# Kernel tuning notes

Hardware: AMD Instinct MI355X
Metric: run time of the kernel (lower is better)

The kernel has to match this reference:

```python
import jax, jax.numpy as jnp
import numpy as np
from jax import lax

IN_CHANNELS = 4
STEPS_IN_ITR = 3


def one_step_ltm(x, T):
    # x: [B, H, W]; T: [B, 10, H, W] (9 stencil weight planes + bias plane)
    B, H, W = x.shape
    xp = jnp.pad(x, ((0, 0), (1, 1), (1, 1)))
    out = T[:, 9]
    k = 0
    # original ordering: X0..X2 scan row-offset with col-offset 0, X3..X5 col 1, X6..X8 col 2
    for dj in range(3):
        for di in range(3):
            out = out + xp[:, di:di + H, dj:dj + W] * T[:, k]
            k += 1
    return out


def setup_inputs() -> dict:
    key = jax.random.key(0)
    k1, k2, k3 = jax.random.split(key, 3)
    B, Tt, C, H, W = 8, 16, 1, 512, 512
    x = jax.random.uniform(k1, (B, Tt, C, H, W), dtype=jnp.float32)
    # stand-in unet: 3x3 SAME conv, in_channels -> 10
    W_unet = jax.random.normal(k2, (10, IN_CHANNELS, 3, 3), dtype=jnp.float32) * 0.1
    b_unet = jax.random.normal(k3, (10,), dtype=jnp.float32) * 0.1
    return {"x": x, "W_unet": W_unet, "b_unet": b_unet}


def reference(x, W_unet, b_unet):
    B, Tt, C, H, W = x.shape
    x_in = x[:, -IN_CHANNELS:, 0]  # [B, in_channels, H, W]
    T = lax.conv_general_dilated(
        x_in, W_unet, window_strides=(1, 1), padding='SAME',
        dimension_numbers=('NCHW', 'OIHW', 'NCHW')) + b_unet[None, :, None, None]

    xt0 = one_step_ltm(x[:, -1, 0], T)  # stored at t=0 WITHOUT sigmoid (as in original)

    def body(xt, _):
        for _j in range(STEPS_IN_ITR):
            xt = one_step_ltm(xt, T)
            xt = jax.nn.sigmoid(one_step_ltm(xt, T))
        return xt, xt

    _, xs = lax.scan(body, xt0, None, length=Tt - 1)  # [Tt-1, B, H, W]
    seq = jnp.concatenate([xt0[None], xs], axis=0)     # [Tt, B, H, W]
    seq = jnp.transpose(seq, (1, 0, 2, 3))             # [B, Tt, H, W]
    xout = jnp.zeros((B, Tt, C, H, W), dtype=x.dtype).at[:, :, 0].set(seq)
    return xout
```

## Files before the change

### kernel.cpp

```cpp
#include <hip/hip_runtime.h>
#include <hip/hip_fp16.h>
#include <math.h>

#define Bd 8
#define Td 16
#define Hd 512
#define Wd 512
#define HWc (Hd * Wd)
#define NPIX (Bd * HWc)

#define VTW 128
#define VTH 16
#define VRW 130
#define VRH 18
#define VP  132
#define VTHR 512

#define WCR 128
#define WCC 64
#define WH  6
#define WTR 140
#define WTC 76
#define WLP 77
#define WTHR 1024
#define WRPG 11
#define WNG 13

__global__ __launch_bounds__(VTHR, 4)
void conv_step0_kernel(const float* __restrict__ x,
                       const float* __restrict__ Wu,
                       const float* __restrict__ bu,
                       __half2* __restrict__ T,
                       float* __restrict__ out) {
    __shared__ __align__(16) float sX[4][VRH][VP];

    int bx  = blockIdx.x;
    int b   = bx >> 7;
    int rem = bx & 127;
    int by  = rem >> 2;
    int bc  = rem & 3;
    int i0  = by * VTH;
    int j0  = bc * VTW;

    const float* xb = x + ((size_t)b * Td + 12) * HWc;
    int tid = threadIdx.x;

    for (int idx = tid; idx < 4 * VRH * VRW; idx += VTHR) {
        int ch = idx / (VRH * VRW);
        int r2 = idx - ch * (VRH * VRW);
        int r  = r2 / VRW;
        int c  = r2 - r * VRW;
        int gi = i0 + r - 1, gj = j0 + c - 1;
        float v = 0.0f;
        if ((unsigned)gi < (unsigned)Hd && (unsigned)gj < (unsigned)Wd)
            v = xb[(size_t)ch * HWc + gi * Wd + gj];
        sX[ch][r][c] = v;
    }
    __syncthreads();

    int tx = tid & 63;
    int ty = tid >> 6;

    float t00[10], t01[10], t10[10], t11[10];
    #pragma unroll
    for (int o = 0; o < 10; ++o) {
        float bv = bu[o];
        t00[o] = bv; t01[o] = bv; t10[o] = bv; t11[o] = bv;
    }

    float w[4][4];
    #pragma unroll
    for (int ch = 0; ch < 4; ++ch) {
        #pragma unroll
        for (int rr = 0; rr < 4; ++rr) {
            const float* rp = &sX[ch][2 * ty + rr][2 * tx];
            float2 a  = *(const float2*)rp;
            float2 b2 = *(const float2*)(rp + 2);
            w[rr][0] = a.x; w[rr][1] = a.y; w[rr][2] = b2.x; w[rr][3] = b2.y;
        }
        #pragma unroll
        for (int kh = 0; kh < 3; ++kh) {
            #pragma unroll
            for (int o = 0; o < 10; ++o) {
                float wt0 = Wu[((o * 4 + ch) * 3 + kh) * 3 + 0];
                float wt1 = Wu[((o * 4 + ch) * 3 + kh) * 3 + 1];
                float wt2 = Wu[((o * 4 + ch) * 3 + kh) * 3 + 2];
                t00[o] += w[kh][0] * wt0 + w[kh][1] * wt1 + w[kh][2] * wt2;
                t01[o] += w[kh][1] * wt0 + w[kh][2] * wt1 + w[kh][3] * wt2;
                t10[o] += w[kh + 1][0] * wt0 + w[kh + 1][1] * wt1 + w[kh + 1][2] * wt2;
                t11[o] += w[kh + 1][1] * wt0 + w[kh + 1][2] * wt1 + w[kh + 1][3] * wt2;
            }
        }
    }

    int gi0 = i0 + 2 * ty;
    int gj0 = j0 + 2 * tx;
    size_t pix0 = (size_t)gi0 * Wd + gj0;
    size_t pix1 = pix0 + Wd;
    __half2* Tb = T + (size_t)b * 5 * HWc;
    #pragma unroll
    for (int q = 0; q < 5; ++q) {
        __half2 a0 = __floats2half2_rn(t00[2 * q], t00[2 * q + 1]);
        __half2 a1 = __floats2half2_rn(t01[2 * q], t01[2 * q + 1]);
        __half2 b0 = __floats2half2_rn(t10[2 * q], t10[2 * q + 1]);
        __half2 b1 = __floats2half2_rn(t11[2 * q], t11[2 * q + 1]);
        uint2 p0, p1;
        p0.x = *(unsigned*)&a0; p0.y = *(unsigned*)&a1;
        p1.x = *(unsigned*)&b0; p1.y = *(unsigned*)&b1;
        *(uint2*)(Tb + (size_t)q * HWc + pix0) = p0;
        *(uint2*)(Tb + (size_t)q * HWc + pix1) = p1;
    }

    float o00 = t00[9], o01 = t01[9], o10 = t10[9], o11 = t11[9];
    #pragma unroll
    for (int dj = 0; dj < 3; ++dj)
        #pragma unroll
        for (int di = 0; di < 3; ++di) {
            int k = dj * 3 + di;
            o00 += w[di][dj]         * t00[k];
            o01 += w[di][dj + 1]     * t01[k];
            o10 += w[di + 1][dj]     * t10[k];
            o11 += w[di + 1][dj + 1] * t11[k];
        }
    float* ob = out + (size_t)b * Td * HWc;
    float2 v0; v0.x = o00; v0.y = o01;
    float2 v1; v1.x = o10; v1.y = o11;
    *(float2*)(ob + pix0) = v0;
    *(float2*)(ob + pix1) = v1;
}

__global__ __launch_bounds__(WTHR, 2)
void fused6_wide_kernel(const float* __restrict__ xin,
                        const __half2* __restrict__ T,
                        float* __restrict__ xout) {
    __shared__ float sA[WTR * WLP];
    __shared__ float sB[WTR * WLP];

    int tile = blockIdx.x;
    int b  = tile >> 5;
    int tr = (tile >> 3) & 3;
    int tc = tile & 7;
    int ri = tr * WCR - WH;
    int rj = tc * WCC - WH;

    const float* xb = xin + (size_t)b * Td * HWc;
    const __half2* Tb = T + (size_t)b * 5 * HWc;
    int tid = threadIdx.x;

    for (int idx = tid; idx < WTR * WTC; idx += WTHR) {
        int r = idx / WTC, c = idx - r * WTC;
        int gi = ri + r, gj = rj + c;
        float v = 0.0f;
        if ((unsigned)gi < (unsigned)Hd && (unsigned)gj < (unsigned)Wd)
            v = xb[gi * Wd + gj];
        sA[r * WLP + c] = v;
    }
    for (int idx = tid; idx < 2 * WTC; idx += WTHR) {
        int r = (idx < WTC) ? 0 : (WTR - 1);
        int c = (idx < WTC) ? idx : idx - WTC;
        sB[r * WLP + c] = 0.0f;
    }
    for (int idx = tid; idx < 2 * WTR; idx += WTHR) {
        int r = (idx < WTR) ? idx : idx - WTR;
        int c = (idx < WTR) ? 0 : (WTC - 1);
        sB[r * WLP + c] = 0.0f;
    }

    int g  = tid / WTC;
    int c  = tid - g * WTC;
    int rs = 1 + g * WRPG;
    bool colint = (c >= 1) && (c <= WTC - 2);
    bool active = (g < WNG) && colint;
    int  gj     = rj + c;
    bool colin  = (unsigned)gj < (unsigned)Wd;

    __half2 treg[WRPG][5];
    #pragma unroll
    for (int jj = 0; jj < WRPG; ++jj) {
        int r  = rs + jj;
        int gi = ri + r;
        bool ok = active && (r <= WTR - 2) && ((unsigned)gi < (unsigned)Hd) && colin;
        #pragma unroll
        for (int q = 0; q < 5; ++q)
            treg[jj][q] = ok ? Tb[(size_t)q * HWc + gi * Wd + gj]
                             : __floats2half2_rn(0.0f, 0.0f);
    }
    __syncthreads();

    float* cur = sA;
    float* nxt = sB;

    #pragma unroll
    for (int s = 1; s <= 6; ++s) {
        if (active) {
            float w00 = cur[(rs - 1) * WLP + c - 1];
            float w01 = cur[(rs - 1) * WLP + c];
            float w02 = cur[(rs - 1) * WLP + c + 1];
            float w10 = cur[rs * WLP + c - 1];
            float w11 = cur[rs * WLP + c];
            float w12 = cur[rs * WLP + c + 1];
            #pragma unroll
            for (int jj = 0; jj < WRPG; ++jj) {
                int r  = rs + jj;
                int r2 = (r + 1 <= WTR - 1) ? (r + 1) : (WTR - 1);
                float w20 = cur[r2 * WLP + c - 1];
                float w21 = cur[r2 * WLP + c];
                float w22 = cur[r2 * WLP + c + 1];

                float2 p0 = __half22float2(treg[jj][0]);
                float2 p1 = __half22float2(treg[jj][1]);
                float2 p2 = __half22float2(treg[jj][2]);
                float2 p3 = __half22float2(treg[jj][3]);
                float2 p4 = __half22float2(treg[jj][4]);

                float a = p4.y
                        + w00 * p0.x + w10 * p0.y + w20 * p1.x
                        + w01 * p1.y + w11 * p2.x + w21 * p2.y
                        + w02 * p3.x + w12 * p3.y + w22 * p4.x;
                if ((s & 1) == 0) a = 1.0f / (1.0f + __expf(-a));

                int gi = ri + r;
                bool rowok = (r <= WTR - 2);
                bool inimg = ((unsigned)gi < (unsigned)Hd) && colin;
                if (rowok) nxt[r * WLP + c] = inimg ? a : 0.0f;

                w00 = w10; w01 = w11; w02 = w12;
                w10 = w20; w11 = w21; w12 = w22;
            }
        }
        __syncthreads();
        float* tmp = cur; cur = nxt; nxt = tmp;
    }

    float* ob = xout + (size_t)b * Td * HWc;
    for (int idx = tid; idx < WCR * WCC; idx += WTHR) {
        int rr = idx >> 6, cc = idx & 63;
        ob[(ri + WH + rr) * Wd + (rj + WH + cc)] = cur[(WH + rr) * WLP + (WH + cc)];
    }
}

extern "C" void kernel_launch(void* const* d_in, const int* in_sizes, int n_in,
                              void* d_out, int out_size, void* d_ws, size_t ws_size,
                              hipStream_t stream) {
    const float* x  = (const float*)d_in[0];
    const float* Wu = (const float*)d_in[1];
    const float* bu = (const float*)d_in[2];
    float* out = (float*)d_out;
    __half2* T = (__half2*)d_ws;

    conv_step0_kernel<<<1024, VTHR, 0, stream>>>(x, Wu, bu, T, out);

    for (int t = 1; t < Td; ++t)
        fused6_wide_kernel<<<256, WTHR, 0, stream>>>(out + (size_t)(t - 1) * HWc, T,
                                                     out + (size_t)t * HWc);
}
```

Measured before the change: 546.8 us.

## Add register-resident lane-shuffle stencil kernel with mixed-precision FMA

```diff
diff --git a/kernel.cpp b/kernel.cpp
--- a/kernel.cpp
+++ b/kernel.cpp
@@ -25,6 +25,44 @@
 #define WTHR 1024
 #define WRPG 11
 #define WNG 13
+
+#define KCR 64
+#define KCC 52
+#define KH  6
+#define KTR 76
+#define KTC 64
+#define KG  7
+#define KR  11
+#define KTHR (KG * 64)
+
+#define FMAMIX_LO(acc, wv, hv) \
+    asm("v_fma_mix_f32 %0, %1, %2, %0 op_sel:[0,0,0] op_sel_hi:[0,1,0]" \
+        : "+v"(acc) : "v"(wv), "v"(hv))
+#define FMAMIX_HI(acc, wv, hv) \
+    asm("v_fma_mix_f32 %0, %1, %2, %0 op_sel:[0,1,0] op_sel_hi:[0,1,0]" \
+        : "+v"(acc) : "v"(wv), "v"(hv))
+
+__device__ __forceinline__ float hi_half_f32(unsigned h) {
+    __half2 hh = *(__half2*)&h;
+    return __half2float(__high2half(hh));
+}
+
+__device__ __forceinline__ float lane_left(float v) {
+#if __has_builtin(__builtin_amdgcn_mov_dpp)
+    return __int_as_float(__builtin_amdgcn_mov_dpp(__float_as_int(v),
+                                                   0x138, 0xf, 0xf, true));
+#else
+    return __shfl_up(v, 1);
+#endif
+}
+__device__ __forceinline__ float lane_right(float v) {
+#if __has_builtin(__builtin_amdgcn_mov_dpp)
+    return __int_as_float(__builtin_amdgcn_mov_dpp(__float_as_int(v),
+                                                   0x130, 0xf, 0xf, true));
+#else
+    return __shfl_down(v, 1);
+#endif
+}
 
 __global__ __launch_bounds__(VTHR, 4)
 void conv_step0_kernel(const float* __restrict__ x,
@@ -129,6 +167,112 @@
     *(float2*)(ob + pix1) = v1;
 }
 
+__global__ __launch_bounds__(KTHR, 2)
+void fused6_lane_kernel(const float* __restrict__ xin,
+                        const __half2* __restrict__ T,
+                        float* __restrict__ xout) {
+    __shared__ float bndF[2][KG][64];
+    __shared__ float bndL[2][KG][64];
+
+    int tile = blockIdx.x;
+    int b   = tile / 80;
+    int rem = tile - b * 80;
+    int tr  = rem / 10;
+    int tc  = rem - tr * 10;
+    int ri  = tr * KCR - KH;
+    int rj  = tc * KCC - KH;
+
+    int tid  = threadIdx.x;
+    int g    = tid >> 6;
+    int lane = tid & 63;
+
+    int  gj     = rj + lane;
+    bool colin  = (unsigned)gj < (unsigned)Wd;
+    bool lanein = (lane >= 1) && (lane <= KTC - 2);
+    int  gjc    = min(max(gj, 0), Wd - 1);
+
+    int rs = 1 + g * KR;
+
+    const float* xb = xin + (size_t)b * Td * HWc;
+    const __half2* Tb = T + (size_t)b * 5 * HWc;
+
+    float xw[KR + 2];
+    #pragma unroll
+    for (int k = 0; k < KR + 2; ++k) {
+        int row = rs - 1 + k;
+        int gi  = ri + row;
+        bool in = ((unsigned)gi < (unsigned)Hd) && colin && (row <= KTR - 1);
+        int gic = min(max(gi, 0), Hd - 1);
+        float v = xb[gic * Wd + gjc];
+        xw[k] = in ? v : 0.0f;
+    }
+
+    unsigned treg[KR][5];
+    #pragma unroll
+    for (int j = 0; j < KR; ++j) {
+        int gi  = ri + rs + j;
+        int gic = min(max(gi, 0), Hd - 1);
+        const unsigned* tp = (const unsigned*)(Tb + gic * Wd + gjc);
+        #pragma unroll
+        for (int q = 0; q < 5; ++q)
+            treg[j][q] = tp[(size_t)q * HWc];
+    }
+
+    int p = 0;
+    #pragma unroll
+    for (int s = 1; s <= 6; ++s) {
+        float pC = xw[0], pL = lane_left(pC), pR = lane_right(pC);
+        float cC = xw[1], cL = lane_left(cC), cR = lane_right(cC);
+        #pragma unroll
+        for (int j = 1; j <= KR; ++j) {
+            float nC = xw[j + 1];
+            float nL = lane_left(nC);
+            float nR = lane_right(nC);
+            unsigned h0 = treg[j - 1][0], h1 = treg[j - 1][1],
+                     h2 = treg[j - 1][2], h3 = treg[j - 1][3],
+                     h4 = treg[j - 1][4];
+            float a = hi_half_f32(h4);
+            FMAMIX_LO(a, pL, h0);
+            FMAMIX_HI(a, cL, h0);
+            FMAMIX_LO(a, nL, h1);
+            FMAMIX_HI(a, pC, h1);
+            FMAMIX_LO(a, cC, h2);
+            FMAMIX_HI(a, nC, h2);
+            FMAMIX_LO(a, pR, h3);
+            FMAMIX_HI(a, cR, h3);
+            FMAMIX_LO(a, nR, h4);
+            if ((s & 1) == 0) a = 1.0f / (1.0f + __expf(-a));
+
+            int row = rs + j - 1;
+            int gi  = ri + row;
+            bool okpix = ((unsigned)gi < (unsigned)Hd) && colin;
+            bool upd   = (row <= KTR - 2) && lanein;
+            float val  = okpix ? a : 0.0f;
+            xw[j] = upd ? val : xw[j];
+
+            pL = cL; pC = cC; pR = cR;
+            cL = nL; cC = nC; cR = nR;
+        }
+        bndF[p][g][lane] = xw[1];
+        bndL[p][g][lane] = xw[KR];
+        __syncthreads();
+        if (g > 0)      xw[0]      = bndL[p][g - 1][lane];
+        if (g < KG - 1) xw[KR + 1] = bndF[p][g + 1][lane];
+        p ^= 1;
+    }
+
+    float* ob = xout + (size_t)b * Td * HWc;
+    bool storec = (lane >= KH) && (lane <= KTC - 1 - KH) && colin;
+    #pragma unroll
+    for (int j = 1; j <= KR; ++j) {
+        int row = rs + j - 1;
+        if (row >= KH && row <= KTR - 1 - KH) {
+            int gi = ri + row;
+            if (storec) ob[gi * Wd + gj] = xw[j];
+        }
+    }
+}
+
 __global__ __launch_bounds__(WTHR, 2)
 void fused6_wide_kernel(const float* __restrict__ xin,
                         const __half2* __restrict__ T,
@@ -174,16 +318,18 @@
     int  gj     = rj + c;
     bool colin  = (unsigned)gj < (unsigned)Wd;
 
-    __half2 treg[WRPG][5];
+    unsigned treg[WRPG][5];
     #pragma unroll
     for (int jj = 0; jj < WRPG; ++jj) {
         int r  = rs + jj;
         int gi = ri + r;
         bool ok = active && (r <= WTR - 2) && ((unsigned)gi < (unsigned)Hd) && colin;
         #pragma unroll
-        for (int q = 0; q < 5; ++q)
-            treg[jj][q] = ok ? Tb[(size_t)q * HWc + gi * Wd + gj]
-                             : __floats2half2_rn(0.0f, 0.0f);
+        for (int q = 0; q < 5; ++q) {
+            unsigned v = 0u;
+            if (ok) v = *(const unsigned*)(Tb + (size_t)q * HWc + gi * Wd + gj);
+            treg[jj][q] = v;
+        }
     }
     __syncthreads();
 
@@ -207,16 +353,18 @@
                 float w21 = cur[r2 * WLP + c];
                 float w22 = cur[r2 * WLP + c + 1];
 
-                float2 p0 = __half22float2(treg[jj][0]);
-                float2 p1 = __half22float2(treg[jj][1]);
-                float2 p2 = __half22float2(treg[jj][2]);
-                float2 p3 = __half22float2(treg[jj][3]);
-                float2 p4 = __half22float2(treg[jj][4]);
-
-                float a = p4.y
-                        + w00 * p0.x + w10 * p0.y + w20 * p1.x
-                        + w01 * p1.y + w11 * p2.x + w21 * p2.y
-                        + w02 * p3.x + w12 * p3.y + w22 * p4.x;
+                unsigned h0 = treg[jj][0], h1 = treg[jj][1], h2 = treg[jj][2],
+                         h3 = treg[jj][3], h4 = treg[jj][4];
+                float a = hi_half_f32(h4);
+                FMAMIX_LO(a, w00, h0);
+                FMAMIX_HI(a, w10, h0);
+                FMAMIX_LO(a, w20, h1);
+                FMAMIX_HI(a, w01, h1);
+                FMAMIX_LO(a, w11, h2);
+                FMAMIX_HI(a, w21, h2);
+                FMAMIX_LO(a, w02, h3);
+                FMAMIX_HI(a, w12, h3);
+                FMAMIX_LO(a, w22, h4);
                 if ((s & 1) == 0) a = 1.0f / (1.0f + __expf(-a));
 
                 int gi = ri + r;
@@ -250,7 +398,17 @@
 
     conv_step0_kernel<<<1024, VTHR, 0, stream>>>(x, Wu, bu, T, out);
 
-    for (int t = 1; t < Td; ++t)
-        fused6_wide_kernel<<<256, WTHR, 0, stream>>>(out + (size_t)(t - 1) * HWc, T,
-                                                     out + (size_t)t * HWc);
-}
+    hipFuncAttributes attr;
+    hipError_t qe = hipFuncGetAttributes(&attr, (const void*)fused6_lane_kernel);
+    bool useLane = (qe == hipSuccess) && (attr.localSizeBytes == 0);
+
+    if (useLane) {
+        for (int t = 1; t < Td; ++t)
+            fused6_lane_kernel<<<640, KTHR, 0, stream>>>(
+                out + (size_t)(t - 1) * HWc, T, out + (size_t)t * HWc);
+    } else {
+        for (int t = 1; t < Td; ++t)
+            fused6_wide_kernel<<<256, WTHR, 0, stream>>>(
+                out + (size_t)(t - 1) * HWc, T, out + (size_t)t * HWc);
+    }
+}
```

Measured after the change: 532.9 us. -2.5%, faster.
